# Performance work log

Measured on AMD Instinct MI355X. Metric: run time of the kernel, lower is better.

Reference implementation:

```python
import jax, jax.numpy as jnp
import numpy as np

N = 1024      # nodes
IN = 64       # input_dim
H = 128       # hidden_dim
L = 4         # num graph layers
HEADS = 4     # MHA heads


def setup_inputs() -> dict:
    key = jax.random.key(0)
    ks = jax.random.split(key, 12)
    s = lambda k, shape: (jax.random.normal(k, shape, dtype=jnp.float32) * 0.05)
    z = lambda shape: jnp.zeros(shape, jnp.float32)
    return {
        "x": jax.random.normal(ks[0], (N, IN), dtype=jnp.float32),
        "emb_W": s(ks[1], (IN, H)), "emb_b": z((H,)),
        "ln_g": jnp.ones((H,), jnp.float32), "ln_b": z((H,)),
        "edge_W1": s(ks[2], (2 * H, H)), "edge_b1": z((H,)),
        "edge_W2": s(ks[3], (H, 1)), "edge_b2": z((1,)),
        "gc_W": s(ks[4], (L, H, H)), "gc_b": z((L, H)),
        "in_proj_W": s(ks[5], (3 * H, H)), "in_proj_b": z((3 * H,)),
        "out_proj_W": s(ks[6], (H, H)), "out_proj_b": z((H,)),
        "out_W": s(ks[7], (H, 6)), "out_b": z((6,)),
    }


def reference(x, emb_W, emb_b, ln_g, ln_b, edge_W1, edge_b1, edge_W2, edge_b2,
              gc_W, gc_b, in_proj_W, in_proj_b, out_proj_W, out_proj_b,
              out_W, out_b):
    # node embedding: Linear -> LayerNorm -> ReLU
    h = x @ emb_W + emb_b
    mu = h.mean(-1, keepdims=True)
    var = ((h - mu) ** 2).mean(-1, keepdims=True)
    h = (h - mu) * jax.lax.rsqrt(var + 1e-5) * ln_g + ln_b
    h = jax.nn.relu(h)

    n, Hd = h.shape
    # dynamic graph: edge MLP on concat(x_i, x_j) for all pairs, batched.
    # cat([x_i, x_j]) @ W1 == x_i @ W1[:H] + x_j @ W1[H:]
    a = h @ edge_W1[:Hd]          # [n, H]
    b = h @ edge_W1[Hd:]          # [n, H]
    e = jax.nn.relu(a[:, None, :] + b[None, :, :] + edge_b1)   # [n, n, H]
    adj = jax.nn.sigmoid(jnp.einsum('ijh,ho->ijo', e, edge_W2)[..., 0] + edge_b2[0])
    adj = adj * (1.0 - jnp.eye(n, dtype=adj.dtype))             # no self-edges

    # physics-informed graph conv layers: adj @ (h @ W) + b
    for l in range(gc_W.shape[0]):
        h = adj @ (h @ gc_W[l]) + gc_b[l]

    # MultiheadAttention (self-attention, seq=n, batch=1)
    d = Hd // HEADS
    qkv = h @ in_proj_W.T + in_proj_b
    q, k, v = jnp.split(qkv, 3, axis=-1)
    q = q.reshape(n, HEADS, d).transpose(1, 0, 2)   # [h, n, d]
    k = k.reshape(n, HEADS, d).transpose(1, 0, 2)
    v = v.reshape(n, HEADS, d).transpose(1, 0, 2)
    scale = 1.0 / np.sqrt(d).astype(np.float32)
    attn = jax.nn.softmax(jnp.einsum('hnd,hmd->hnm', q, k) * scale, axis=-1)
    o = jnp.einsum('hnm,hmd->hnd', attn, v).transpose(1, 0, 2).reshape(n, Hd)
    h = o @ out_proj_W.T + out_proj_b

    # pooled head + per-metric activations
    out = h.mean(0) @ out_W + out_b                 # [6]
    sig = jax.nn.sigmoid(out)
    return jnp.stack([sig[0], jax.nn.relu(out[1]), sig[2], sig[3], sig[4], sig[5]])
```

## Files before the change

### kernel.cpp

```cpp
#include <hip/hip_runtime.h>
#include <math.h>

#define NN 1024
#define IN_DIM 64
#define H 128
#define NL 4
#define HEADS 4
#define DH 32
#define KSPLIT 8
#define NSPLIT 16

__global__ __launch_bounds__(128) void k_embed(const float* __restrict__ x,
        const float* __restrict__ embW, const float* __restrict__ embB,
        const float* __restrict__ lng, const float* __restrict__ lnb,
        const float* __restrict__ eW1, const float* __restrict__ eb1,
        const float* __restrict__ gcW0,
        const float* __restrict__ inW, const float* __restrict__ outW,
        float* __restrict__ Wt_in, float* __restrict__ Wt_out,
        float* __restrict__ aM, float* __restrict__ bM, float* __restrict__ g0) {
    __shared__ float xs[IN_DIM];
    __shared__ float hs[H];
    __shared__ float red[H];
    int i = blockIdx.x, t = threadIdx.x;
    int gidx = i * 128 + t;
    if (gidx < 49152) {
        Wt_in[gidx] = inW[(gidx % 384) * 128 + gidx / 384];
    } else if (gidx < 65536) {
        int i2 = gidx - 49152;
        Wt_out[i2] = outW[(i2 % 128) * 128 + i2 / 128];
    }
    if (t < IN_DIM) xs[t] = x[i * IN_DIM + t];
    __syncthreads();
    float acc = embB[t];
    #pragma unroll 8
    for (int k = 0; k < IN_DIM; ++k) acc = fmaf(xs[k], embW[k * H + t], acc);
    red[t] = acc; __syncthreads();
    for (int s = 64; s > 0; s >>= 1) { if (t < s) red[t] += red[t + s]; __syncthreads(); }
    float mu = red[0] * (1.f / H);
    __syncthreads();
    float d = acc - mu;
    red[t] = d * d; __syncthreads();
    for (int s = 64; s > 0; s >>= 1) { if (t < s) red[t] += red[t + s]; __syncthreads(); }
    float var = red[0] * (1.f / H);
    float hv = d * rsqrtf(var + 1e-5f) * lng[t] + lnb[t];
    hv = fmaxf(hv, 0.f);
    hs[t] = hv;
    __syncthreads();
    float aa = eb1[t], bb = 0.f, gg = 0.f;
    #pragma unroll 8
    for (int k = 0; k < H; ++k) {
        float hk = hs[k];
        aa = fmaf(hk, eW1[k * H + t], aa);
        bb = fmaf(hk, eW1[(H + k) * H + t], bb);
        gg = fmaf(hk, gcW0[k * H + t], gg);
    }
    aM[i * H + t] = aa;
    bM[i * H + t] = bb;
    g0[i * H + t] = gg;
}

#define AT 32
__global__ __launch_bounds__(256) void k_adj(const float* __restrict__ aM, const float* __restrict__ bM,
        const float* __restrict__ w2, const float* __restrict__ eb2p, float* __restrict__ adj) {
    __shared__ float as_[AT][H + 4];
    __shared__ float bst[H][AT + 4];
    __shared__ float w2s[H];
    int i0 = blockIdx.y * AT, j0 = blockIdx.x * AT;
    int t = threadIdx.x;
    for (int idx = t; idx < AT * H; idx += 256) {
        int r = idx >> 7, c = idx & 127;
        as_[r][c] = aM[(i0 + r) * H + c];
        bst[c][r] = bM[(j0 + r) * H + c];
    }
    if (t < H) w2s[t] = w2[t];
    __syncthreads();
    int ti = t >> 3, tjg = t & 7;
    float a0 = 0.f, a1 = 0.f, a2 = 0.f, a3 = 0.f;
    const float eb2 = eb2p[0];
    #pragma unroll 4
    for (int h = 0; h < H; ++h) {
        float av = as_[ti][h];
        float4 bv = *(const float4*)&bst[h][tjg * 4];
        float wh = w2s[h];
        a0 = fmaf(fmaxf(av + bv.x, 0.f), wh, a0);
        a1 = fmaf(fmaxf(av + bv.y, 0.f), wh, a1);
        a2 = fmaf(fmaxf(av + bv.z, 0.f), wh, a2);
        a3 = fmaf(fmaxf(av + bv.w, 0.f), wh, a3);
    }
    int i = i0 + ti, jb = j0 + tjg * 4;
    float4 ov;
    ov.x = (i == jb + 0) ? 0.f : 1.f / (1.f + __expf(-(a0 + eb2)));
    ov.y = (i == jb + 1) ? 0.f : 1.f / (1.f + __expf(-(a1 + eb2)));
    ov.z = (i == jb + 2) ? 0.f : 1.f / (1.f + __expf(-(a2 + eb2)));
    ov.w = (i == jb + 3) ? 0.f : 1.f / (1.f + __expf(-(a3 + eb2)));
    *(float4*)&adj[(size_t)i * NN + jb] = ov;
}

__global__ __launch_bounds__(128) void k_spmm(const float* __restrict__ adj, const float* __restrict__ g,
        float* __restrict__ partial) {
    __shared__ float adjs[16][65];
    int r0 = blockIdx.x * 16;
    int j0 = blockIdx.y * 64;
    int t = threadIdx.x;
    #pragma unroll
    for (int it = 0; it < 2; ++it) {
        int idx = t + it * 128;
        int r = idx >> 4, jg = idx & 15;
        float4 av = *(const float4*)&adj[(size_t)(r0 + r) * NN + j0 + jg * 4];
        adjs[r][jg * 4 + 0] = av.x; adjs[r][jg * 4 + 1] = av.y;
        adjs[r][jg * 4 + 2] = av.z; adjs[r][jg * 4 + 3] = av.w;
    }
    __syncthreads();
    int rg = t >> 5, cg = t & 31;
    int c0 = cg * 4;
    float acc[4][4] = {};
    #pragma unroll 4
    for (int jj = 0; jj < 64; ++jj) {
        float ga[4];
        *(float4*)ga = *(const float4*)&g[(j0 + jj) * H + c0];
        #pragma unroll
        for (int r = 0; r < 4; ++r) {
            float av = adjs[rg * 4 + r][jj];
            #pragma unroll
            for (int c = 0; c < 4; ++c) acc[r][c] = fmaf(av, ga[c], acc[r][c]);
        }
    }
    #pragma unroll
    for (int r = 0; r < 4; ++r) {
        float4 ov = {acc[r][0], acc[r][1], acc[r][2], acc[r][3]};
        *(float4*)&partial[((size_t)blockIdx.y * NN + r0 + rg * 4 + r) * H + c0] = ov;
    }
}

__global__ __launch_bounds__(128) void k_redmat128(const float* __restrict__ partial,
        const float* __restrict__ bias, const float* __restrict__ W, float* __restrict__ outM) {
    __shared__ float s[H];
    int i = blockIdx.x, t = threadIdx.x;
    float v = bias[t];
    #pragma unroll
    for (int p = 0; p < NSPLIT; ++p) v += partial[(size_t)p * NN * H + i * H + t];
    s[t] = v;
    __syncthreads();
    float acc = 0.f;
    #pragma unroll 8
    for (int k = 0; k < H; ++k) acc = fmaf(s[k], W[k * H + t], acc);
    outM[i * H + t] = acc;
}

__global__ __launch_bounds__(384) void k_redmat384(const float* __restrict__ partial,
        const float* __restrict__ bias, const float* __restrict__ W,
        const float* __restrict__ bias2, float* __restrict__ outM) {
    __shared__ float s[H];
    int i = blockIdx.x, t = threadIdx.x;
    if (t < H) {
        float v = bias[t];
        #pragma unroll
        for (int p = 0; p < NSPLIT; ++p) v += partial[(size_t)p * NN * H + i * H + t];
        s[t] = v;
    }
    __syncthreads();
    float acc = bias2[t];
    #pragma unroll 8
    for (int k = 0; k < H; ++k) acc = fmaf(s[k], W[k * 384 + t], acc);
    outM[i * 384 + t] = acc;
}

__global__ __launch_bounds__(256) void k_attn_part(const float* __restrict__ qkv,
        float* __restrict__ opart, float* __restrict__ mpart, float* __restrict__ lpart) {
    __shared__ float kob[4][32][36];
    __shared__ float qT[32][36];
    __shared__ float pT[128][36];
    __shared__ float marr[32], larr[32];
    float* kT = &kob[0][0][0];
    const int t = threadIdx.x;
    const int head = blockIdx.y, kp = blockIdx.z;
    const int i0 = blockIdx.x * 32, j0 = kp * 128;
    const int qoff = head * DH, koff = H + head * DH, voff = 2 * H + head * DH;
    const float scale = 0.17677669529663687f;
    {
        int qi = t >> 3, dg = t & 7;
        float4 qv = *(const float4*)&qkv[(i0 + qi) * 384 + qoff + dg * 4];
        qT[dg * 4 + 0][qi] = qv.x * scale;
        qT[dg * 4 + 1][qi] = qv.y * scale;
        qT[dg * 4 + 2][qi] = qv.z * scale;
        qT[dg * 4 + 3][qi] = qv.w * scale;
    }
    #pragma unroll
    for (int it = 0; it < 4; ++it) {
        int idx = t + it * 256;
        int j = idx >> 3, dg = idx & 7;
        float4 kv = *(const float4*)&qkv[(j0 + j) * 384 + koff + dg * 4];
        kT[(dg * 4 + 0) * 132 + j] = kv.x;
        kT[(dg * 4 + 1) * 132 + j] = kv.y;
        kT[(dg * 4 + 2) * 132 + j] = kv.z;
        kT[(dg * 4 + 3) * 132 + j] = kv.w;
    }
    __syncthreads();
    const int tq = t >> 5, tj = t & 31;
    float s[4][4] = {};
    #pragma unroll
    for (int kk = 0; kk < DH; ++kk) {
        float qa[4], ka[4];
        *(float4*)qa = *(float4*)&qT[kk][tq * 4];
        *(float4*)ka = *(float4*)&kT[kk * 132 + tj * 4];
        #pragma unroll
        for (int a = 0; a < 4; ++a)
            #pragma unroll
            for (int b = 0; b < 4; ++b) s[a][b] = fmaf(qa[a], ka[b], s[a][b]);
    }
    #pragma unroll
    for (int a = 0; a < 4; ++a) {
        float mm = fmaxf(fmaxf(s[a][0], s[a][1]), fmaxf(s[a][2], s[a][3]));
        #pragma unroll
        for (int off = 16; off > 0; off >>= 1) mm = fmaxf(mm, __shfl_xor(mm, off));
        float ll = 0.f;
        #pragma unroll
        for (int b = 0; b < 4; ++b) { s[a][b] = __expf(s[a][b] - mm); ll += s[a][b]; }
        #pragma unroll
        for (int off = 16; off > 0; off >>= 1) ll += __shfl_xor(ll, off);
        if (tj == 0) { marr[tq * 4 + a] = mm; larr[tq * 4 + a] = ll; }
    }
    #pragma unroll
    for (int b = 0; b < 4; ++b)
        #pragma unroll
        for (int a = 0; a < 4; ++a) pT[tj * 4 + b][tq * 4 + a] = s[a][b];
    __syncthreads();
    const int qg = t >> 5, dg = (t >> 2) & 7, st = t & 3;
    float o[4][4] = {};
    #pragma unroll 4
    for (int jj = 0; jj < 32; ++jj) {
        int j = st * 32 + jj;
        float pa[4], va[4];
        *(float4*)pa = *(float4*)&pT[j][qg * 4];
        *(float4*)va = *(const float4*)&qkv[(j0 + j) * 384 + voff + dg * 4];
        #pragma unroll
        for (int a = 0; a < 4; ++a)
            #pragma unroll
            for (int b = 0; b < 4; ++b) o[a][b] = fmaf(pa[a], va[b], o[a][b]);
    }
    #pragma unroll
    for (int a = 0; a < 4; ++a)
        #pragma unroll
        for (int b = 0; b < 4; ++b) kob[st][qg * 4 + a][dg * 4 + b] = o[a][b];
    __syncthreads();
    {
        int q = t >> 3, d0 = (t & 7) * 4;
        float r0[4], r1[4], r2[4], r3[4];
        *(float4*)r0 = *(float4*)&kob[0][q][d0];
        *(float4*)r1 = *(float4*)&kob[1][q][d0];
        *(float4*)r2 = *(float4*)&kob[2][q][d0];
        *(float4*)r3 = *(float4*)&kob[3][q][d0];
        float4 ov;
        ov.x = (r0[0] + r1[0]) + (r2[0] + r3[0]);
        ov.y = (r0[1] + r1[1]) + (r2[1] + r3[1]);
        ov.z = (r0[2] + r1[2]) + (r2[2] + r3[2]);
        ov.w = (r0[3] + r1[3]) + (r2[3] + r3[3]);
        int pidx = head * KSPLIT + kp;
        *(float4*)&opart[((size_t)pidx * NN + i0 + q) * DH + d0] = ov;
        if (t < 32) {
            mpart[pidx * NN + i0 + t] = marr[t];
            lpart[pidx * NN + i0 + t] = larr[t];
        }
    }
}

__global__ __launch_bounds__(128) void k_mergeproj(const float* __restrict__ opart,
        const float* __restrict__ mpart, const float* __restrict__ lpart,
        const float* __restrict__ Wt_out, const float* __restrict__ bias,
        float* __restrict__ h2) {
    __shared__ float s[H];
    int row = blockIdx.x, t = threadIdx.x;
    int head = t >> 5, d = t & 31;
    float mv[KSPLIT];
    float M = -1e30f;
    #pragma unroll
    for (int p = 0; p < KSPLIT; ++p) {
        mv[p] = mpart[(head * KSPLIT + p) * NN + row];
        M = fmaxf(M, mv[p]);
    }
    float L = 0.f, o = 0.f;
    #pragma unroll
    for (int p = 0; p < KSPLIT; ++p) {
        float w = __expf(mv[p] - M);
        L = fmaf(lpart[(head * KSPLIT + p) * NN + row], w, L);
        o = fmaf(opart[((size_t)(head * KSPLIT + p) * NN + row) * DH + d], w, o);
    }
    s[t] = o / L;
    __syncthreads();
    float acc = bias[t];
    #pragma unroll 8
    for (int k = 0; k < H; ++k) acc = fmaf(s[k], Wt_out[k * H + t], acc);
    h2[row * H + t] = acc;
}

__global__ void k_pool1(const float* __restrict__ h2, float* __restrict__ pp) {
    int b = blockIdx.x;
    int t = threadIdx.x;
    int c = t & 127, rg = t >> 7;
    int r0 = b * 32 + rg * 16;
    float s = 0.f;
    #pragma unroll
    for (int r = 0; r < 16; ++r) s += h2[(r0 + r) * H + c];
    pp[(b * 2 + rg) * H + c] = s;
}

__global__ void k_pool2(const float* __restrict__ pp, const float* __restrict__ outW,
        const float* __restrict__ outB, float* __restrict__ out) {
    __shared__ float pooled[H];
    int t = threadIdx.x;
    float s = 0.f;
    #pragma unroll 8
    for (int p = 0; p < 64; ++p) s += pp[p * H + t];
    pooled[t] = s * (1.f / 1024.f);
    __syncthreads();
    if (t < 6) {
        float acc = outB[t];
        for (int c = 0; c < H; ++c) acc = fmaf(pooled[c], outW[c * 6 + t], acc);
        out[t] = (t == 1) ? fmaxf(acc, 0.f) : 1.f / (1.f + expf(-acc));
    }
}

extern "C" void kernel_launch(void* const* d_in, const int* in_sizes, int n_in,
                              void* d_out, int out_size, void* d_ws, size_t ws_size,
                              hipStream_t stream) {
    const float* x       = (const float*)d_in[0];
    const float* emb_W   = (const float*)d_in[1];
    const float* emb_b   = (const float*)d_in[2];
    const float* ln_g    = (const float*)d_in[3];
    const float* ln_b    = (const float*)d_in[4];
    const float* edge_W1 = (const float*)d_in[5];
    const float* edge_b1 = (const float*)d_in[6];
    const float* edge_W2 = (const float*)d_in[7];
    const float* edge_b2 = (const float*)d_in[8];
    const float* gc_W    = (const float*)d_in[9];
    const float* gc_b    = (const float*)d_in[10];
    const float* in_proj_W  = (const float*)d_in[11];
    const float* in_proj_b  = (const float*)d_in[12];
    const float* out_proj_W = (const float*)d_in[13];
    const float* out_proj_b = (const float*)d_in[14];
    const float* out_W   = (const float*)d_in[15];
    const float* out_b   = (const float*)d_in[16];
    float* out = (float*)d_out;

    float* ws = (float*)d_ws;
    float* aM      = ws;
    float* bM      = aM + NN * H;
    float* adj     = bM + NN * H;
    float* g       = adj + NN * NN;
    float* partial = g + NN * H;
    float* qkv     = partial + (size_t)NSPLIT * NN * H;
    float* Wt_in   = qkv + NN * 384;
    float* Wt_out  = Wt_in + 128 * 384;
    float* pp      = Wt_out + 128 * 128;
    float* opart = adj;
    float* mpart = aM;
    float* lpart = aM + 32 * NN;
    float* h2    = g;

    k_embed<<<NN, 128, 0, stream>>>(x, emb_W, emb_b, ln_g, ln_b, edge_W1, edge_b1,
                                    gc_W, in_proj_W, out_proj_W, Wt_in, Wt_out,
                                    aM, bM, g);
    k_adj<<<dim3(NN / AT, NN / AT), 256, 0, stream>>>(aM, bM, edge_W2, edge_b2, adj);

    for (int l = 0; l < NL; ++l) {
        k_spmm<<<dim3(NN / 16, NSPLIT), 128, 0, stream>>>(adj, g, partial);
        if (l < NL - 1)
            k_redmat128<<<NN, 128, 0, stream>>>(partial, gc_b + (size_t)l * H,
                                                gc_W + (size_t)(l + 1) * H * H, g);
        else
            k_redmat384<<<NN, 384, 0, stream>>>(partial, gc_b + (size_t)l * H,
                                                Wt_in, in_proj_b, qkv);
    }

    k_attn_part<<<dim3(NN / 32, HEADS, KSPLIT), 256, 0, stream>>>(qkv, opart, mpart, lpart);
    k_mergeproj<<<NN, 128, 0, stream>>>(opart, mpart, lpart, Wt_out, out_proj_b, h2);
    k_pool1<<<32, 256, 0, stream>>>(h2, pp);
    k_pool2<<<1, 128, 0, stream>>>(pp, out_W, out_b, out);
}
```

Before: 159.3 us.

## Fuse all stages into one persistent kernel with atomic grid barriers

Replaces roughly fourteen separate kernel launches with one persistent kernel of 512 blocks. The stages are separated by software grid barriers built on an atomic counter, and a small init kernel resets the counter first. Each 256-thread block handles two rows or tiles per stage, and the pooling step is now a single-block reduction. The aim is to remove launch overhead and inter-kernel gaps. The cost is spin-wait barriers that depend on all blocks being co-resident, plus a spin timeout that could silently break correctness.

Measured after the change: 622.4 us. +290.8%, slower.

```diff
diff --git a/kernel.cpp b/kernel.cpp
--- a/kernel.cpp
+++ b/kernel.cpp
@@ -2,378 +2,355 @@
 #include <math.h>
 
 #define NN 1024
-#define IN_DIM 64
 #define H 128
 #define NL 4
-#define HEADS 4
-#define DH 32
-#define KSPLIT 8
-#define NSPLIT 16
-
-__global__ __launch_bounds__(128) void k_embed(const float* __restrict__ x,
-        const float* __restrict__ embW, const float* __restrict__ embB,
-        const float* __restrict__ lng, const float* __restrict__ lnb,
-        const float* __restrict__ eW1, const float* __restrict__ eb1,
-        const float* __restrict__ gcW0,
-        const float* __restrict__ inW, const float* __restrict__ outW,
-        float* __restrict__ Wt_in, float* __restrict__ Wt_out,
-        float* __restrict__ aM, float* __restrict__ bM, float* __restrict__ g0) {
-    __shared__ float xs[IN_DIM];
-    __shared__ float hs[H];
-    __shared__ float red[H];
-    int i = blockIdx.x, t = threadIdx.x;
-    int gidx = i * 128 + t;
-    if (gidx < 49152) {
-        Wt_in[gidx] = inW[(gidx % 384) * 128 + gidx / 384];
-    } else if (gidx < 65536) {
-        int i2 = gidx - 49152;
-        Wt_out[i2] = outW[(i2 % 128) * 128 + i2 / 128];
-    }
-    if (t < IN_DIM) xs[t] = x[i * IN_DIM + t];
+#define NBLK 512
+
+struct Params {
+    const float *x, *embW, *embB, *lng, *lnb, *eW1, *eb1, *eW2, *eb2;
+    const float *gcW, *gcb, *inW, *inb, *outPW, *outPb, *outW, *outb;
+    float *aM, *bM, *adj, *g, *partial, *qkv, *Wt_in, *Wt_out;
+    float *opart, *mpart, *lpart, *h2, *out;
+    unsigned *cnt;
+};
+
+union SMem {
+    struct { float xs[2][64]; float red[2][128]; float hs[2][128]; } emb;
+    struct { float as_[32][132]; float bst[128][36]; float w2s[128]; } aj;
+    struct { float adjs[2][16][65]; } sp;
+    struct { float s[2][128]; } rm;
+    struct { float kob[4][32][36]; float qT[32][36]; float pT[128][36];
+             float marr[32]; float larr[32]; } at;
+    struct { float p0[2][128]; } pl;
+};
+
+__global__ void k_init(unsigned* cnt) {
+    if (threadIdx.x == 0) {
+        __hip_atomic_store(cnt, 0u, __ATOMIC_RELEASE, __HIP_MEMORY_SCOPE_AGENT);
+    }
+}
+
+__device__ __forceinline__ void gbar(unsigned* cnt, unsigned target) {
     __syncthreads();
-    float acc = embB[t];
-    #pragma unroll 8
-    for (int k = 0; k < IN_DIM; ++k) acc = fmaf(xs[k], embW[k * H + t], acc);
-    red[t] = acc; __syncthreads();
-    for (int s = 64; s > 0; s >>= 1) { if (t < s) red[t] += red[t + s]; __syncthreads(); }
-    float mu = red[0] * (1.f / H);
+    if (threadIdx.x == 0) {
+        __hip_atomic_fetch_add(cnt, 1u, __ATOMIC_ACQ_REL, __HIP_MEMORY_SCOPE_AGENT);
+        long spins = 0;
+        while (__hip_atomic_load(cnt, __ATOMIC_ACQUIRE, __HIP_MEMORY_SCOPE_AGENT) < target) {
+            __builtin_amdgcn_s_sleep(2);
+            if (++spins > 8000000L) break;
+        }
+    }
     __syncthreads();
-    float d = acc - mu;
-    red[t] = d * d; __syncthreads();
-    for (int s = 64; s > 0; s >>= 1) { if (t < s) red[t] += red[t + s]; __syncthreads(); }
-    float var = red[0] * (1.f / H);
-    float hv = d * rsqrtf(var + 1e-5f) * lng[t] + lnb[t];
-    hv = fmaxf(hv, 0.f);
-    hs[t] = hv;
-    __syncthreads();
-    float aa = eb1[t], bb = 0.f, gg = 0.f;
-    #pragma unroll 8
-    for (int k = 0; k < H; ++k) {
-        float hk = hs[k];
-        aa = fmaf(hk, eW1[k * H + t], aa);
-        bb = fmaf(hk, eW1[(H + k) * H + t], bb);
-        gg = fmaf(hk, gcW0[k * H + t], gg);
-    }
-    aM[i * H + t] = aa;
-    bM[i * H + t] = bb;
-    g0[i * H + t] = gg;
 }
 
-#define AT 32
-__global__ __launch_bounds__(256) void k_adj(const float* __restrict__ aM, const float* __restrict__ bM,
-        const float* __restrict__ w2, const float* __restrict__ eb2p, float* __restrict__ adj) {
-    __shared__ float as_[AT][H + 4];
-    __shared__ float bst[H][AT + 4];
-    __shared__ float w2s[H];
-    int i0 = blockIdx.y * AT, j0 = blockIdx.x * AT;
-    int t = threadIdx.x;
-    for (int idx = t; idx < AT * H; idx += 256) {
-        int r = idx >> 7, c = idx & 127;
-        as_[r][c] = aM[(i0 + r) * H + c];
-        bst[c][r] = bM[(j0 + r) * H + c];
-    }
-    if (t < H) w2s[t] = w2[t];
-    __syncthreads();
-    int ti = t >> 3, tjg = t & 7;
-    float a0 = 0.f, a1 = 0.f, a2 = 0.f, a3 = 0.f;
-    const float eb2 = eb2p[0];
-    #pragma unroll 4
-    for (int h = 0; h < H; ++h) {
-        float av = as_[ti][h];
-        float4 bv = *(const float4*)&bst[h][tjg * 4];
-        float wh = w2s[h];
-        a0 = fmaf(fmaxf(av + bv.x, 0.f), wh, a0);
-        a1 = fmaf(fmaxf(av + bv.y, 0.f), wh, a1);
-        a2 = fmaf(fmaxf(av + bv.z, 0.f), wh, a2);
-        a3 = fmaf(fmaxf(av + bv.w, 0.f), wh, a3);
-    }
-    int i = i0 + ti, jb = j0 + tjg * 4;
-    float4 ov;
-    ov.x = (i == jb + 0) ? 0.f : 1.f / (1.f + __expf(-(a0 + eb2)));
-    ov.y = (i == jb + 1) ? 0.f : 1.f / (1.f + __expf(-(a1 + eb2)));
-    ov.z = (i == jb + 2) ? 0.f : 1.f / (1.f + __expf(-(a2 + eb2)));
-    ov.w = (i == jb + 3) ? 0.f : 1.f / (1.f + __expf(-(a3 + eb2)));
-    *(float4*)&adj[(size_t)i * NN + jb] = ov;
-}
-
-__global__ __launch_bounds__(128) void k_spmm(const float* __restrict__ adj, const float* __restrict__ g,
-        float* __restrict__ partial) {
-    __shared__ float adjs[16][65];
-    int r0 = blockIdx.x * 16;
-    int j0 = blockIdx.y * 64;
-    int t = threadIdx.x;
-    #pragma unroll
-    for (int it = 0; it < 2; ++it) {
-        int idx = t + it * 128;
-        int r = idx >> 4, jg = idx & 15;
-        float4 av = *(const float4*)&adj[(size_t)(r0 + r) * NN + j0 + jg * 4];
-        adjs[r][jg * 4 + 0] = av.x; adjs[r][jg * 4 + 1] = av.y;
-        adjs[r][jg * 4 + 2] = av.z; adjs[r][jg * 4 + 3] = av.w;
-    }
-    __syncthreads();
-    int rg = t >> 5, cg = t & 31;
-    int c0 = cg * 4;
-    float acc[4][4] = {};
-    #pragma unroll 4
-    for (int jj = 0; jj < 64; ++jj) {
-        float ga[4];
-        *(float4*)ga = *(const float4*)&g[(j0 + jj) * H + c0];
-        #pragma unroll
-        for (int r = 0; r < 4; ++r) {
-            float av = adjs[rg * 4 + r][jj];
-            #pragma unroll
-            for (int c = 0; c < 4; ++c) acc[r][c] = fmaf(av, ga[c], acc[r][c]);
-        }
-    }
-    #pragma unroll
-    for (int r = 0; r < 4; ++r) {
-        float4 ov = {acc[r][0], acc[r][1], acc[r][2], acc[r][3]};
-        *(float4*)&partial[((size_t)blockIdx.y * NN + r0 + rg * 4 + r) * H + c0] = ov;
-    }
-}
-
-__global__ __launch_bounds__(128) void k_redmat128(const float* __restrict__ partial,
-        const float* __restrict__ bias, const float* __restrict__ W, float* __restrict__ outM) {
-    __shared__ float s[H];
-    int i = blockIdx.x, t = threadIdx.x;
-    float v = bias[t];
-    #pragma unroll
-    for (int p = 0; p < NSPLIT; ++p) v += partial[(size_t)p * NN * H + i * H + t];
-    s[t] = v;
-    __syncthreads();
-    float acc = 0.f;
-    #pragma unroll 8
-    for (int k = 0; k < H; ++k) acc = fmaf(s[k], W[k * H + t], acc);
-    outM[i * H + t] = acc;
-}
-
-__global__ __launch_bounds__(384) void k_redmat384(const float* __restrict__ partial,
-        const float* __restrict__ bias, const float* __restrict__ W,
-        const float* __restrict__ bias2, float* __restrict__ outM) {
-    __shared__ float s[H];
-    int i = blockIdx.x, t = threadIdx.x;
-    if (t < H) {
-        float v = bias[t];
-        #pragma unroll
-        for (int p = 0; p < NSPLIT; ++p) v += partial[(size_t)p * NN * H + i * H + t];
-        s[t] = v;
-    }
-    __syncthreads();
-    float acc = bias2[t];
-    #pragma unroll 8
-    for (int k = 0; k < H; ++k) acc = fmaf(s[k], W[k * 384 + t], acc);
-    outM[i * 384 + t] = acc;
-}
-
-__global__ __launch_bounds__(256) void k_attn_part(const float* __restrict__ qkv,
-        float* __restrict__ opart, float* __restrict__ mpart, float* __restrict__ lpart) {
-    __shared__ float kob[4][32][36];
-    __shared__ float qT[32][36];
-    __shared__ float pT[128][36];
-    __shared__ float marr[32], larr[32];
-    float* kT = &kob[0][0][0];
-    const int t = threadIdx.x;
-    const int head = blockIdx.y, kp = blockIdx.z;
-    const int i0 = blockIdx.x * 32, j0 = kp * 128;
-    const int qoff = head * DH, koff = H + head * DH, voff = 2 * H + head * DH;
-    const float scale = 0.17677669529663687f;
+__global__ __launch_bounds__(256, 2) void mega(Params P) {
+    __shared__ SMem sm;
+    const int B = blockIdx.x, T = threadIdx.x;
+    const int half = T >> 7, t = T & 127;
+
     {
-        int qi = t >> 3, dg = t & 7;
-        float4 qv = *(const float4*)&qkv[(i0 + qi) * 384 + qoff + dg * 4];
-        qT[dg * 4 + 0][qi] = qv.x * scale;
-        qT[dg * 4 + 1][qi] = qv.y * scale;
-        qT[dg * 4 + 2][qi] = qv.z * scale;
-        qT[dg * 4 + 3][qi] = qv.w * scale;
-    }
-    #pragma unroll
-    for (int it = 0; it < 4; ++it) {
-        int idx = t + it * 256;
-        int j = idx >> 3, dg = idx & 7;
-        float4 kv = *(const float4*)&qkv[(j0 + j) * 384 + koff + dg * 4];
-        kT[(dg * 4 + 0) * 132 + j] = kv.x;
-        kT[(dg * 4 + 1) * 132 + j] = kv.y;
-        kT[(dg * 4 + 2) * 132 + j] = kv.z;
-        kT[(dg * 4 + 3) * 132 + j] = kv.w;
-    }
-    __syncthreads();
-    const int tq = t >> 5, tj = t & 31;
-    float s[4][4] = {};
-    #pragma unroll
-    for (int kk = 0; kk < DH; ++kk) {
-        float qa[4], ka[4];
-        *(float4*)qa = *(float4*)&qT[kk][tq * 4];
-        *(float4*)ka = *(float4*)&kT[kk * 132 + tj * 4];
+        if (T < 128) {
+            int gidx = B * 128 + T;
+            if (gidx < 49152) P.Wt_in[gidx] = P.inW[(gidx % 384) * 128 + gidx / 384];
+            else { int i2 = gidx - 49152; P.Wt_out[i2] = P.outPW[(i2 % 128) * 128 + i2 / 128]; }
+        }
+        int row = B * 2 + half;
+        if (t < 64) sm.emb.xs[half][t] = P.x[row * 64 + t];
+        __syncthreads();
+        float acc = P.embB[t];
+        #pragma unroll 8
+        for (int k = 0; k < 64; ++k) acc = fmaf(sm.emb.xs[half][k], P.embW[k * H + t], acc);
+        sm.emb.red[half][t] = acc; __syncthreads();
+        for (int s = 64; s > 0; s >>= 1) { if (t < s) sm.emb.red[half][t] += sm.emb.red[half][t + s]; __syncthreads(); }
+        float mu = sm.emb.red[half][0] * (1.f / H);
+        __syncthreads();
+        float d = acc - mu;
+        sm.emb.red[half][t] = d * d; __syncthreads();
+        for (int s = 64; s > 0; s >>= 1) { if (t < s) sm.emb.red[half][t] += sm.emb.red[half][t + s]; __syncthreads(); }
+        float var = sm.emb.red[half][0] * (1.f / H);
+        float hv = fmaxf(d * rsqrtf(var + 1e-5f) * P.lng[t] + P.lnb[t], 0.f);
+        sm.emb.hs[half][t] = hv;
+        __syncthreads();
+        float aa = P.eb1[t], bb = 0.f, gg = 0.f;
+        #pragma unroll 8
+        for (int k = 0; k < H; ++k) {
+            float hk = sm.emb.hs[half][k];
+            aa = fmaf(hk, P.eW1[k * H + t], aa);
+            bb = fmaf(hk, P.eW1[(H + k) * H + t], bb);
+            gg = fmaf(hk, P.gcW[k * H + t], gg);
+        }
+        P.aM[row * H + t] = aa; P.bM[row * H + t] = bb; P.g[row * H + t] = gg;
+    }
+    gbar(P.cnt, NBLK * 1);
+
+    for (int tt = 0; tt < 2; ++tt) {
+        __syncthreads();
+        int tile = B * 2 + tt;
+        int i0 = (tile >> 5) * 32, j0 = (tile & 31) * 32;
+        for (int idx = T; idx < 32 * H; idx += 256) {
+            int r = idx >> 7, c = idx & 127;
+            sm.aj.as_[r][c] = P.aM[(i0 + r) * H + c];
+            sm.aj.bst[c][r] = P.bM[(j0 + r) * H + c];
+        }
+        if (T < H) sm.aj.w2s[T] = P.eW2[T];
+        __syncthreads();
+        int ti = T >> 3, tjg = T & 7;
+        float a0 = 0.f, a1 = 0.f, a2 = 0.f, a3 = 0.f;
+        const float eb2 = P.eb2[0];
+        #pragma unroll 4
+        for (int h = 0; h < H; ++h) {
+            float av = sm.aj.as_[ti][h];
+            float4 bv = *(const float4*)&sm.aj.bst[h][tjg * 4];
+            float wh = sm.aj.w2s[h];
+            a0 = fmaf(fmaxf(av + bv.x, 0.f), wh, a0);
+            a1 = fmaf(fmaxf(av + bv.y, 0.f), wh, a1);
+            a2 = fmaf(fmaxf(av + bv.z, 0.f), wh, a2);
+            a3 = fmaf(fmaxf(av + bv.w, 0.f), wh, a3);
+        }
+        int i = i0 + ti, jb = j0 + tjg * 4;
+        float4 ov;
+        ov.x = (i == jb + 0) ? 0.f : 1.f / (1.f + __expf(-(a0 + eb2)));
+        ov.y = (i == jb + 1) ? 0.f : 1.f / (1.f + __expf(-(a1 + eb2)));
+        ov.z = (i == jb + 2) ? 0.f : 1.f / (1.f + __expf(-(a2 + eb2)));
+        ov.w = (i == jb + 3) ? 0.f : 1.f / (1.f + __expf(-(a3 + eb2)));
+        *(float4*)&P.adj[(size_t)i * NN + jb] = ov;
+    }
+    gbar(P.cnt, NBLK * 2);
+
+    for (int l = 0; l < NL; ++l) {
+        {
+            int v = B * 2 + half, rb = v >> 4, p = v & 15;
+            int r0 = rb * 16, j0 = p * 64;
+            #pragma unroll
+            for (int it = 0; it < 2; ++it) {
+                int idx = t + it * 128;
+                int r = idx >> 4, jg = idx & 15;
+                float4 av = *(const float4*)&P.adj[(size_t)(r0 + r) * NN + j0 + jg * 4];
+                sm.sp.adjs[half][r][jg * 4 + 0] = av.x;
+                sm.sp.adjs[half][r][jg * 4 + 1] = av.y;
+                sm.sp.adjs[half][r][jg * 4 + 2] = av.z;
+                sm.sp.adjs[half][r][jg * 4 + 3] = av.w;
+            }
+            __syncthreads();
+            int rg = t >> 5, c0 = (t & 31) * 4;
+            float acc[4][4] = {};
+            #pragma unroll 4
+            for (int jj = 0; jj < 64; ++jj) {
+                float ga[4];
+                *(float4*)ga = *(const float4*)&P.g[(j0 + jj) * H + c0];
+                #pragma unroll
+                for (int r = 0; r < 4; ++r) {
+                    float av = sm.sp.adjs[half][rg * 4 + r][jj];
+                    #pragma unroll
+                    for (int c = 0; c < 4; ++c) acc[r][c] = fmaf(av, ga[c], acc[r][c]);
+                }
+            }
+            #pragma unroll
+            for (int r = 0; r < 4; ++r) {
+                float4 ov = {acc[r][0], acc[r][1], acc[r][2], acc[r][3]};
+                *(float4*)&P.partial[((size_t)p * NN + r0 + rg * 4 + r) * H + c0] = ov;
+            }
+        }
+        gbar(P.cnt, NBLK * (3 + 2 * l));
+        {
+            int row = B * 2 + half;
+            float vv = P.gcb[l * H + t];
+            #pragma unroll
+            for (int p = 0; p < 16; ++p) vv += P.partial[(size_t)p * NN * H + row * H + t];
+            sm.rm.s[half][t] = vv;
+            __syncthreads();
+            if (l < NL - 1) {
+                const float* W = P.gcW + (size_t)(l + 1) * H * H;
+                float acc = 0.f;
+                #pragma unroll 8
+                for (int k = 0; k < H; ++k) acc = fmaf(sm.rm.s[half][k], W[k * H + t], acc);
+                P.g[row * H + t] = acc;
+            } else {
+                #pragma unroll
+                for (int it = 0; it < 3; ++it) {
+                    int c = t + it * 128;
+                    float acc = P.inb[c];
+                    #pragma unroll 8
+                    for (int k = 0; k < H; ++k) acc = fmaf(sm.rm.s[half][k], P.Wt_in[k * 384 + c], acc);
+                    P.qkv[row * 384 + c] = acc;
+                }
+            }
+        }
+        gbar(P.cnt, NBLK * (4 + 2 * l));
+    }
+
+    for (int tt = 0; tt < 2; ++tt) {
+        __syncthreads();
+        int v = B * 2 + tt;
+        int i0 = (v & 31) * 32, head = (v >> 5) & 3, kp = v >> 7, j0 = kp * 128;
+        int qoff = head * 32, koff = 128 + head * 32, voff = 256 + head * 32;
+        float* kT = &sm.at.kob[0][0][0];
+        const float scale = 0.17677669529663687f;
+        {
+            int qi = T >> 3, dg = T & 7;
+            float4 qv = *(const float4*)&P.qkv[(i0 + qi) * 384 + qoff + dg * 4];
+            sm.at.qT[dg * 4 + 0][qi] = qv.x * scale;
+            sm.at.qT[dg * 4 + 1][qi] = qv.y * scale;
+            sm.at.qT[dg * 4 + 2][qi] = qv.z * scale;
+            sm.at.qT[dg * 4 + 3][qi] = qv.w * scale;
+        }
+        #pragma unroll
+        for (int it = 0; it < 4; ++it) {
+            int idx = T + it * 256;
+            int j = idx >> 3, dg = idx & 7;
+            float4 kv = *(const float4*)&P.qkv[(j0 + j) * 384 + koff + dg * 4];
+            kT[(dg * 4 + 0) * 132 + j] = kv.x;
+            kT[(dg * 4 + 1) * 132 + j] = kv.y;
+            kT[(dg * 4 + 2) * 132 + j] = kv.z;
+            kT[(dg * 4 + 3) * 132 + j] = kv.w;
+        }
+        __syncthreads();
+        int tq = T >> 5, tj = T & 31;
+        float s[4][4] = {};
+        #pragma unroll
+        for (int kk = 0; kk < 32; ++kk) {
+            float qa[4], ka[4];
+            *(float4*)qa = *(float4*)&sm.at.qT[kk][tq * 4];
+            *(float4*)ka = *(float4*)&kT[kk * 132 + tj * 4];
+            #pragma unroll
+            for (int a = 0; a < 4; ++a)
+                #pragma unroll
+                for (int b = 0; b < 4; ++b) s[a][b] = fmaf(qa[a], ka[b], s[a][b]);
+        }
+        #pragma unroll
+        for (int a = 0; a < 4; ++a) {
+            float mm = fmaxf(fmaxf(s[a][0], s[a][1]), fmaxf(s[a][2], s[a][3]));
+            #pragma unroll
+            for (int off = 16; off > 0; off >>= 1) mm = fmaxf(mm, __shfl_xor(mm, off));
+            float ll = 0.f;
+            #pragma unroll
+            for (int b = 0; b < 4; ++b) { s[a][b] = __expf(s[a][b] - mm); ll += s[a][b]; }
+            #pragma unroll
+            for (int off = 16; off > 0; off >>= 1) ll += __shfl_xor(ll, off);
+            if (tj == 0) { sm.at.marr[tq * 4 + a] = mm; sm.at.larr[tq * 4 + a] = ll; }
+        }
+        #pragma unroll
+        for (int b = 0; b < 4; ++b)
+            #pragma unroll
+            for (int a = 0; a < 4; ++a) sm.at.pT[tj * 4 + b][tq * 4 + a] = s[a][b];
+        __syncthreads();
+        int qg = T >> 5, dg2 = (T >> 2) & 7, st = T & 3;
+        float o[4][4] = {};
+        #pragma unroll 4
+        for (int jj = 0; jj < 32; ++jj) {
+            int j = st * 32 + jj;
+            float pa[4], va[4];
+            *(float4*)pa = *(float4*)&sm.at.pT[j][qg * 4];
+            *(float4*)va = *(const float4*)&P.qkv[(j0 + j) * 384 + voff + dg2 * 4];
+            #pragma unroll
+            for (int a = 0; a < 4; ++a)
+                #pragma unroll
+                for (int b = 0; b < 4; ++b) o[a][b] = fmaf(pa[a], va[b], o[a][b]);
+        }
+        __syncthreads();
         #pragma unroll
         for (int a = 0; a < 4; ++a)
             #pragma unroll
-            for (int b = 0; b < 4; ++b) s[a][b] = fmaf(qa[a], ka[b], s[a][b]);
-    }
-    #pragma unroll
-    for (int a = 0; a < 4; ++a) {
-        float mm = fmaxf(fmaxf(s[a][0], s[a][1]), fmaxf(s[a][2], s[a][3]));
-        #pragma unroll
-        for (int off = 16; off > 0; off >>= 1) mm = fmaxf(mm, __shfl_xor(mm, off));
-        float ll = 0.f;
-        #pragma unroll
-        for (int b = 0; b < 4; ++b) { s[a][b] = __expf(s[a][b] - mm); ll += s[a][b]; }
-        #pragma unroll
-        for (int off = 16; off > 0; off >>= 1) ll += __shfl_xor(ll, off);
-        if (tj == 0) { marr[tq * 4 + a] = mm; larr[tq * 4 + a] = ll; }
-    }
-    #pragma unroll
-    for (int b = 0; b < 4; ++b)
-        #pragma unroll
-        for (int a = 0; a < 4; ++a) pT[tj * 4 + b][tq * 4 + a] = s[a][b];
-    __syncthreads();
-    const int qg = t >> 5, dg = (t >> 2) & 7, st = t & 3;
-    float o[4][4] = {};
-    #pragma unroll 4
-    for (int jj = 0; jj < 32; ++jj) {
-        int j = st * 32 + jj;
-        float pa[4], va[4];
-        *(float4*)pa = *(float4*)&pT[j][qg * 4];
-        *(float4*)va = *(const float4*)&qkv[(j0 + j) * 384 + voff + dg * 4];
-        #pragma unroll
-        for (int a = 0; a < 4; ++a)
-            #pragma unroll
-            for (int b = 0; b < 4; ++b) o[a][b] = fmaf(pa[a], va[b], o[a][b]);
-    }
-    #pragma unroll
-    for (int a = 0; a < 4; ++a)
-        #pragma unroll
-        for (int b = 0; b < 4; ++b) kob[st][qg * 4 + a][dg * 4 + b] = o[a][b];
-    __syncthreads();
+            for (int b = 0; b < 4; ++b) sm.at.kob[st][qg * 4 + a][dg2 * 4 + b] = o[a][b];
+        __syncthreads();
+        {
+            int q = T >> 3, d0 = (T & 7) * 4;
+            float r0[4], r1[4], r2[4], r3[4];
+            *(float4*)r0 = *(float4*)&sm.at.kob[0][q][d0];
+            *(float4*)r1 = *(float4*)&sm.at.kob[1][q][d0];
+            *(float4*)r2 = *(float4*)&sm.at.kob[2][q][d0];
+            *(float4*)r3 = *(float4*)&sm.at.kob[3][q][d0];
+            float4 ov;
+            ov.x = (r0[0] + r1[0]) + (r2[0] + r3[0]);
+            ov.y = (r0[1] + r1[1]) + (r2[1] + r3[1]);
+            ov.z = (r0[2] + r1[2]) + (r2[2] + r3[2]);
+            ov.w = (r0[3] + r1[3]) + (r2[3] + r3[3]);
+            int pidx = head * 8 + kp;
+            *(float4*)&P.opart[((size_t)pidx * NN + i0 + q) * 32 + d0] = ov;
+            if (T < 32) {
+                P.mpart[pidx * NN + i0 + T] = sm.at.marr[T];
+                P.lpart[pidx * NN + i0 + T] = sm.at.larr[T];
+            }
+        }
+    }
+    gbar(P.cnt, NBLK * 11);
+
     {
-        int q = t >> 3, d0 = (t & 7) * 4;
-        float r0[4], r1[4], r2[4], r3[4];
-        *(float4*)r0 = *(float4*)&kob[0][q][d0];
-        *(float4*)r1 = *(float4*)&kob[1][q][d0];
-        *(float4*)r2 = *(float4*)&kob[2][q][d0];
-        *(float4*)r3 = *(float4*)&kob[3][q][d0];
-        float4 ov;
-        ov.x = (r0[0] + r1[0]) + (r2[0] + r3[0]);
-        ov.y = (r0[1] + r1[1]) + (r2[1] + r3[1]);
-        ov.z = (r0[2] + r1[2]) + (r2[2] + r3[2]);
-        ov.w = (r0[3] + r1[3]) + (r2[3] + r3[3]);
-        int pidx = head * KSPLIT + kp;
-        *(float4*)&opart[((size_t)pidx * NN + i0 + q) * DH + d0] = ov;
-        if (t < 32) {
-            mpart[pidx * NN + i0 + t] = marr[t];
-            lpart[pidx * NN + i0 + t] = larr[t];
-        }
-    }
-}
-
-__global__ __launch_bounds__(128) void k_mergeproj(const float* __restrict__ opart,
-        const float* __restrict__ mpart, const float* __restrict__ lpart,
-        const float* __restrict__ Wt_out, const float* __restrict__ bias,
-        float* __restrict__ h2) {
-    __shared__ float s[H];
-    int row = blockIdx.x, t = threadIdx.x;
-    int head = t >> 5, d = t & 31;
-    float mv[KSPLIT];
-    float M = -1e30f;
-    #pragma unroll
-    for (int p = 0; p < KSPLIT; ++p) {
-        mv[p] = mpart[(head * KSPLIT + p) * NN + row];
-        M = fmaxf(M, mv[p]);
-    }
-    float L = 0.f, o = 0.f;
-    #pragma unroll
-    for (int p = 0; p < KSPLIT; ++p) {
-        float w = __expf(mv[p] - M);
-        L = fmaf(lpart[(head * KSPLIT + p) * NN + row], w, L);
-        o = fmaf(opart[((size_t)(head * KSPLIT + p) * NN + row) * DH + d], w, o);
-    }
-    s[t] = o / L;
-    __syncthreads();
-    float acc = bias[t];
-    #pragma unroll 8
-    for (int k = 0; k < H; ++k) acc = fmaf(s[k], Wt_out[k * H + t], acc);
-    h2[row * H + t] = acc;
-}
-
-__global__ void k_pool1(const float* __restrict__ h2, float* __restrict__ pp) {
-    int b = blockIdx.x;
-    int t = threadIdx.x;
-    int c = t & 127, rg = t >> 7;
-    int r0 = b * 32 + rg * 16;
-    float s = 0.f;
-    #pragma unroll
-    for (int r = 0; r < 16; ++r) s += h2[(r0 + r) * H + c];
-    pp[(b * 2 + rg) * H + c] = s;
-}
-
-__global__ void k_pool2(const float* __restrict__ pp, const float* __restrict__ outW,
-        const float* __restrict__ outB, float* __restrict__ out) {
-    __shared__ float pooled[H];
-    int t = threadIdx.x;
-    float s = 0.f;
-    #pragma unroll 8
-    for (int p = 0; p < 64; ++p) s += pp[p * H + t];
-    pooled[t] = s * (1.f / 1024.f);
-    __syncthreads();
-    if (t < 6) {
-        float acc = outB[t];
-        for (int c = 0; c < H; ++c) acc = fmaf(pooled[c], outW[c * 6 + t], acc);
-        out[t] = (t == 1) ? fmaxf(acc, 0.f) : 1.f / (1.f + expf(-acc));
+        int row = B * 2 + half;
+        int hd = t >> 5, d = t & 31;
+        float mv[8], M = -1e30f;
+        #pragma unroll
+        for (int p = 0; p < 8; ++p) {
+            mv[p] = P.mpart[(hd * 8 + p) * NN + row];
+            M = fmaxf(M, mv[p]);
+        }
+        float L = 0.f, o = 0.f;
+        #pragma unroll
+        for (int p = 0; p < 8; ++p) {
+            float w = __expf(mv[p] - M);
+            L = fmaf(P.lpart[(hd * 8 + p) * NN + row], w, L);
+            o = fmaf(P.opart[((size_t)(hd * 8 + p) * NN + row) * 32 + d], w, o);
+        }
+        sm.rm.s[half][t] = o / L;
+        __syncthreads();
+        float acc = P.outPb[t];
+        #pragma unroll 8
+        for (int k = 0; k < H; ++k) acc = fmaf(sm.rm.s[half][k], P.Wt_out[k * H + t], acc);
+        P.h2[row * H + t] = acc;
+    }
+    gbar(P.cnt, NBLK * 12);
+
+    if (B == 0) {
+        float s = 0.f;
+        int rbase = half * 512;
+        #pragma unroll 8
+        for (int r = 0; r < 512; ++r) s += P.h2[(rbase + r) * H + t];
+        sm.pl.p0[half][t] = s;
+        __syncthreads();
+        if (T < 128) sm.pl.p0[0][t] = (sm.pl.p0[0][t] + sm.pl.p0[1][t]) * (1.f / 1024.f);
+        __syncthreads();
+        if (T < 6) {
+            float acc = P.outb[T];
+            #pragma unroll 8
+            for (int c = 0; c < H; ++c) acc = fmaf(sm.pl.p0[0][c], P.outW[c * 6 + T], acc);
+            P.out[T] = (T == 1) ? fmaxf(acc, 0.f) : 1.f / (1.f + __expf(-acc));
+        }
     }
 }
 
 extern "C" void kernel_launch(void* const* d_in, const int* in_sizes, int n_in,
                               void* d_out, int out_size, void* d_ws, size_t ws_size,
                               hipStream_t stream) {
-    const float* x       = (const float*)d_in[0];
-    const float* emb_W   = (const float*)d_in[1];
-    const float* emb_b   = (const float*)d_in[2];
-    const float* ln_g    = (const float*)d_in[3];
-    const float* ln_b    = (const float*)d_in[4];
-    const float* edge_W1 = (const float*)d_in[5];
-    const float* edge_b1 = (const float*)d_in[6];
-    const float* edge_W2 = (const float*)d_in[7];
-    const float* edge_b2 = (const float*)d_in[8];
-    const float* gc_W    = (const float*)d_in[9];
-    const float* gc_b    = (const float*)d_in[10];
-    const float* in_proj_W  = (const float*)d_in[11];
-    const float* in_proj_b  = (const float*)d_in[12];
-    const float* out_proj_W = (const float*)d_in[13];
-    const float* out_proj_b = (const float*)d_in[14];
-    const float* out_W   = (const float*)d_in[15];
-    const float* out_b   = (const float*)d_in[16];
-    float* out = (float*)d_out;
-
     float* ws = (float*)d_ws;
     float* aM      = ws;
     float* bM      = aM + NN * H;
     float* adj     = bM + NN * H;
-    float* g       = adj + NN * NN;
+    float* g       = adj + (size_t)NN * NN;
     float* partial = g + NN * H;
-    float* qkv     = partial + (size_t)NSPLIT * NN * H;
-    float* Wt_in   = qkv + NN * 384;
-    float* Wt_out  = Wt_in + 128 * 384;
-    float* pp      = Wt_out + 128 * 128;
-    float* opart = adj;
-    float* mpart = aM;
-    float* lpart = aM + 32 * NN;
-    float* h2    = g;
-
-    k_embed<<<NN, 128, 0, stream>>>(x, emb_W, emb_b, ln_g, ln_b, edge_W1, edge_b1,
-                                    gc_W, in_proj_W, out_proj_W, Wt_in, Wt_out,
-                                    aM, bM, g);
-    k_adj<<<dim3(NN / AT, NN / AT), 256, 0, stream>>>(aM, bM, edge_W2, edge_b2, adj);
-
-    for (int l = 0; l < NL; ++l) {
-        k_spmm<<<dim3(NN / 16, NSPLIT), 128, 0, stream>>>(adj, g, partial);
-        if (l < NL - 1)
-            k_redmat128<<<NN, 128, 0, stream>>>(partial, gc_b + (size_t)l * H,
-                                                gc_W + (size_t)(l + 1) * H * H, g);
-        else
-            k_redmat384<<<NN, 384, 0, stream>>>(partial, gc_b + (size_t)l * H,
-                                                Wt_in, in_proj_b, qkv);
-    }
-
-    k_attn_part<<<dim3(NN / 32, HEADS, KSPLIT), 256, 0, stream>>>(qkv, opart, mpart, lpart);
-    k_mergeproj<<<NN, 128, 0, stream>>>(opart, mpart, lpart, Wt_out, out_proj_b, h2);
-    k_pool1<<<32, 256, 0, stream>>>(h2, pp);
-    k_pool2<<<1, 128, 0, stream>>>(pp, out_W, out_b, out);
+    float* qkv     = partial + (size_t)16 * NN * H;
+    float* Wt_in   = qkv + (size_t)NN * 384;
+    float* Wt_out  = Wt_in + 49152;
+    unsigned* cnt  = (unsigned*)(Wt_out + 16384 + 256);
+
+    Params p;
+    p.x = (const float*)d_in[0];
+    p.embW = (const float*)d_in[1];  p.embB = (const float*)d_in[2];
+    p.lng = (const float*)d_in[3];   p.lnb = (const float*)d_in[4];
+    p.eW1 = (const float*)d_in[5];   p.eb1 = (const float*)d_in[6];
+    p.eW2 = (const float*)d_in[7];   p.eb2 = (const float*)d_in[8];
+    p.gcW = (const float*)d_in[9];   p.gcb = (const float*)d_in[10];
+    p.inW = (const float*)d_in[11];  p.inb = (const float*)d_in[12];
+    p.outPW = (const float*)d_in[13]; p.outPb = (const float*)d_in[14];
+    p.outW = (const float*)d_in[15]; p.outb = (const float*)d_in[16];
+    p.aM = aM; p.bM = bM; p.adj = adj; p.g = g; p.partial = partial;
+    p.qkv = qkv; p.Wt_in = Wt_in; p.Wt_out = Wt_out;
+    p.opart = adj;
+    p.mpart = aM;
+    p.lpart = aM + 32 * NN;
+    p.h2    = g;
+    p.out = (float*)d_out;
+    p.cnt = cnt;
+
+    k_init<<<1, 64, 0, stream>>>(cnt);
+    mega<<<dim3(NBLK), dim3(256), 0, stream>>>(p);
 }
```
